# Performance work log

Measured on AMD Instinct MI355X. Metric: run time of the kernel, lower is better.

Reference implementation:

```python
import jax, jax.numpy as jnp
import numpy as np


def _log_g(x):
    # log of g(x) = where(x>=0, x+0.5, sigmoid(x)), computed stably in log-space
    return jnp.where(x >= 0, jnp.log(jax.nn.relu(x) + 0.5), -jax.nn.softplus(-x))


def setup_inputs() -> dict:
    key = jax.random.key(0)
    k1, k2, k3, k4, k5 = jax.random.split(key, 5)
    B, T, D, E = 4, 4096, 1024, 2048  # batch, seq, dim, exp_dim (expansion 2.0)
    x = jax.random.normal(k1, (B, T, D), dtype=jnp.float32)
    log_h_0 = jax.random.normal(k2, (B, 1, E), dtype=jnp.float32)
    # torch Linear(dim, 2*exp_dim): store transposed weight [D, 2E] for x @ w_f
    w_f = jax.random.normal(k3, (D, 2 * E), dtype=jnp.float32) * (1.0 / np.sqrt(D))
    b_f = jax.random.normal(k4, (2 * E,), dtype=jnp.float32) * 0.01
    # torch Linear(exp_dim, dim, bias=False): stored as [E, D] for h_t @ w_down
    w_down = jax.random.normal(k5, (E, D), dtype=jnp.float32) * (1.0 / np.sqrt(E))
    return {"x": x, "log_h_0": log_h_0, "w_f": w_f, "b_f": b_f, "w_down": w_down}


def reference(x, log_h_0, w_f, b_f, w_down):
    # fused gate/candidate projection: [B,T,2E]
    proj = jnp.einsum("btd,de->bte", x, w_f) + b_f
    k, h_x = jnp.split(proj, 2, axis=-1)  # each [B,T,E]
    log_z = -jax.nn.softplus(-k)          # log sigmoid(k)
    log_coeffs = -jax.nn.softplus(k)      # log (1 - sigmoid(k))
    log_tilde_h = _log_g(h_x)
    # prepend initial state: log_values [B,T+1,E]
    log_values = jnp.concatenate([log_h_0, log_tilde_h + log_z], axis=1)
    # a_star = pad(cumsum(log_coeffs), one leading zero along time) -> [B,T+1,E]
    a_star = jnp.pad(jnp.cumsum(log_coeffs, axis=1), ((0, 0), (1, 0), (0, 0)))
    # log-space parallel scan
    log_h = a_star + jax.lax.cumlogsumexp(log_values - a_star, axis=1)
    h_t = jnp.exp(log_h)[:, 1:]  # [B,T,E]
    h = jnp.einsum("bte,ed->btd", h_t, w_down)  # down projection (dropout p=0 -> identity)
    return h, jnp.log(h_t[:, 2:-1:3])
```

## Files before the change

kernel.cpp:

```cpp
#include <hip/hip_runtime.h>
#include <cstdint>
#include <cstddef>

typedef __attribute__((ext_vector_type(4))) float f32x4;
typedef __attribute__((ext_vector_type(8))) short short8;

__device__ __forceinline__ unsigned short f2bf(float f) {
  unsigned int u = __float_as_uint(f);
  u += 0x7fffu + ((u >> 16) & 1u);
  return (unsigned short)(u >> 16);
}
__device__ __forceinline__ float bf2f(unsigned short h) {
  return __uint_as_float(((unsigned int)h) << 16);
}

__device__ __forceinline__ void gload16(const unsigned short* g, unsigned short* l) {
  __builtin_amdgcn_global_load_lds(
      (const __attribute__((address_space(1))) void*)g,
      (__attribute__((address_space(3))) void*)l, 16, 0, 0);
}

__global__ __launch_bounds__(256) void k_cast(const float* __restrict__ src,
                                              unsigned short* __restrict__ hi) {
  size_t i = ((size_t)blockIdx.x * 256 + threadIdx.x) * 4;
  float4 v = *(const float4*)(src + i);
  *(ushort4*)(hi + i) = make_ushort4(f2bf(v.x), f2bf(v.y), f2bf(v.z), f2bf(v.w));
}

__global__ __launch_bounds__(256) void k_transpose(const float* __restrict__ src,
                                                   unsigned short* __restrict__ hi,
                                                   int R, int C) {
  __shared__ float tile[32][33];
  int tx = threadIdx.x & 31, ty = threadIdx.x >> 5;
  int c0 = blockIdx.x * 32, r0 = blockIdx.y * 32;
#pragma unroll
  for (int i = 0; i < 4; ++i)
    tile[ty + 8 * i][tx] = src[(size_t)(r0 + ty + 8 * i) * C + (c0 + tx)];
  __syncthreads();
#pragma unroll
  for (int i = 0; i < 4; ++i) {
    float v = tile[tx][ty + 8 * i];
    hi[(size_t)(c0 + ty + 8 * i) * R + (r0 + tx)] = f2bf(v);
  }
}

template<bool BF16OUT>
__global__ __launch_bounds__(512, 2) void k_gemm(const unsigned short* __restrict__ A,
                                                 const unsigned short* __restrict__ B,
                                                 void* __restrict__ Cv, int M, int N, int K) {
  __shared__ unsigned short lds[65536];
  const int tid = threadIdx.x, wave = tid >> 6, lane = tid & 63;
  const size_t row0 = (size_t)blockIdx.x * 256;
  const size_t col0 = (size_t)blockIdx.y * 256;
  const int wr = wave >> 2, wc = wave & 3;
  const int r16 = lane & 15;
  const int ksw = (lane >> 4) ^ ((r16 >> 1) & 3);
  const int aoff = (wr * 128 + r16) * 32 + ksw * 8;
  const int boff = 8192 + (wc * 64 + r16) * 32 + ksw * 8;
  const int gchunk = (tid & 3) ^ ((tid >> 3) & 3);

  f32x4 acc[8][4];
#pragma unroll
  for (int i = 0; i < 8; ++i)
#pragma unroll
    for (int j = 0; j < 4; ++j) acc[i][j] = (f32x4){0.f, 0.f, 0.f, 0.f};

  auto SREG = [&](int b, int arr, int inst, int kt) {
    const unsigned short* src = arr ? B : A;
    size_t grow = (arr ? col0 : row0) + (size_t)(inst * 128 + (tid >> 2));
    gload16(src + grow * (size_t)K + (size_t)(kt * 32 + gchunk * 8),
            &lds[(b << 14) + arr * 8192 + inst * 4096 + wave * 512]);
  };

#pragma unroll
  for (int t = 0; t < 3; ++t) {
    SREG(t, 0, 0, t); SREG(t, 0, 1, t);
    SREG(t, 1, 0, t); SREG(t, 1, 1, t);
  }

  const int nT = K >> 5;
  for (int u = 0; u < nT; ++u) {
    const unsigned short* buf = &lds[(u & 3) << 14];
    const int sb = (u + 3) & 3;
    const bool pf = (u + 3 < nT);
    const int rem = nT - 1 - u;
    if (rem >= 2)      asm volatile("s_waitcnt vmcnt(8)" ::: "memory");
    else if (rem == 1) asm volatile("s_waitcnt vmcnt(4)" ::: "memory");
    else               asm volatile("s_waitcnt vmcnt(0)" ::: "memory");
    asm volatile("s_barrier" ::: "memory");
    short8 a4[4], b4[4];
#pragma unroll
    for (int nb = 0; nb < 4; ++nb)
      b4[nb] = *(const short8*)&buf[boff + nb * 512];
#pragma unroll
    for (int mb = 0; mb < 4; ++mb)
      a4[mb] = *(const short8*)&buf[aoff + mb * 512];
    if (pf) { SREG(sb, 0, 0, u + 3); SREG(sb, 1, 0, u + 3); }
    __builtin_amdgcn_s_setprio(1);
#pragma unroll
    for (int mb = 0; mb < 4; ++mb)
#pragma unroll
      for (int nb = 0; nb < 4; ++nb)
        acc[mb][nb] = __builtin_amdgcn_mfma_f32_16x16x32_bf16(a4[mb], b4[nb], acc[mb][nb], 0, 0, 0);
    __builtin_amdgcn_s_setprio(0);
#pragma unroll
    for (int mb = 0; mb < 4; ++mb)
      a4[mb] = *(const short8*)&buf[aoff + (4 + mb) * 512];
    if (pf) { SREG(sb, 0, 1, u + 3); SREG(sb, 1, 1, u + 3); }
    __builtin_amdgcn_s_setprio(1);
#pragma unroll
    for (int mb = 0; mb < 4; ++mb)
#pragma unroll
      for (int nb = 0; nb < 4; ++nb)
        acc[4 + mb][nb] = __builtin_amdgcn_mfma_f32_16x16x32_bf16(a4[mb], b4[nb], acc[4 + mb][nb], 0, 0, 0);
    __builtin_amdgcn_s_setprio(0);
  }

#pragma unroll
  for (int m = 0; m < 8; ++m)
#pragma unroll
    for (int n = 0; n < 4; ++n) {
      size_t row = row0 + wr * 128 + m * 16 + (lane >> 4) * 4;
      size_t col = col0 + wc * 64 + n * 16 + r16;
      if (BF16OUT) {
        unsigned short* C = (unsigned short*)Cv;
#pragma unroll
        for (int r = 0; r < 4; ++r) C[(row + r) * (size_t)N + col] = f2bf(acc[m][n][r]);
      } else {
        float* C = (float*)Cv;
#pragma unroll
        for (int r = 0; r < 4; ++r) C[(row + r) * (size_t)N + col] = acc[m][n][r];
      }
    }
}

#define SB 4
#define ST 4096
#define SE 2048
#define CHUNK 64
#define NCHUNK 64
#define NCHAIN (SB * SE)

__device__ __forceinline__ void transform_lin(float k, float hx, float& c, float& v) {
  float e = __expf(-k);
  float r = __builtin_amdgcn_rcpf(1.f + e);
  c = e * r;
  float e2 = __expf(-hx);
  float sg = __builtin_amdgcn_rcpf(1.f + e2);
  float g = (hx >= 0.f) ? (hx + 0.5f) : sg;
  v = r * g;
}

__global__ __launch_bounds__(256) void k_scan1(const unsigned short* __restrict__ proj,
                                               const float* __restrict__ bfv,
                                               float* __restrict__ Ac,
                                               float* __restrict__ Bc) {
  int idx = blockIdx.x * 256 + threadIdx.x;
  int e = idx & (SE - 1), b = (idx >> 11) & 3, c = idx >> 13;
  const float bk = bfv[e], bh = bfv[SE + e];
  float A = 1.f, S = 0.f;
  size_t base = ((size_t)(b * ST + c * CHUNK) * (2 * SE)) + e;
  for (int i = 0; i < CHUNK; ++i) {
    float cc, vv;
    transform_lin(bf2f(proj[base]) + bk, bf2f(proj[base + SE]) + bh, cc, vv);
    A *= cc;
    S = fmaf(cc, S, vv);
    base += 2 * SE;
  }
  int chain = b * SE + e;
  Ac[(size_t)c * NCHAIN + chain] = A;
  Bc[(size_t)c * NCHAIN + chain] = S;
}

__global__ __launch_bounds__(256) void k_scan2(const float* __restrict__ lh0,
                                               const float* __restrict__ Ac,
                                               const float* __restrict__ Bc,
                                               float* __restrict__ Hin) {
  int chain = blockIdx.x * 256 + threadIdx.x;
  float H = __expf(lh0[chain]);
  for (int c = 0; c < NCHUNK; ++c) {
    Hin[(size_t)c * NCHAIN + chain] = H;
    H = fmaf(Ac[(size_t)c * NCHAIN + chain], H, Bc[(size_t)c * NCHAIN + chain]);
  }
}

__global__ __launch_bounds__(256) void k_scan3(const unsigned short* __restrict__ proj,
                                               const float* __restrict__ bfv,
                                               const float* __restrict__ Hin,
                                               unsigned short* __restrict__ ht,
                                               float* __restrict__ out2) {
  int idx = blockIdx.x * 256 + threadIdx.x;
  int e = idx & (SE - 1), b = (idx >> 11) & 3, c = idx >> 13;
  const float bk = bfv[e], bh = bfv[SE + e];
  float S = Hin[(size_t)c * NCHAIN + b * SE + e];
  size_t base = ((size_t)(b * ST + c * CHUNK) * (2 * SE)) + e;
  int t = c * CHUNK;
  size_t hto = ((size_t)(b * ST + t) * SE) + e;
  for (int i = 0; i < CHUNK; ++i, ++t) {
    float cc, vv;
    transform_lin(bf2f(proj[base]) + bk, bf2f(proj[base + SE]) + bh, cc, vv);
    S = fmaf(cc, S, vv);
    ht[hto] = f2bf(S);
    if (t >= 2 && ((t - 2) % 3) == 0) {
      int j = (t - 2) / 3;
      out2[((size_t)b * 1365 + j) * SE + e] = __logf(S);
    }
    base += 2 * SE;
    hto += SE;
  }
}

extern "C" void kernel_launch(void* const* d_in, const int* in_sizes, int n_in,
                              void* d_out, int out_size, void* d_ws, size_t ws_size,
                              hipStream_t stream) {
  const float* x   = (const float*)d_in[0];
  const float* lh0 = (const float*)d_in[1];
  const float* wf  = (const float*)d_in[2];
  const float* bfv = (const float*)d_in[3];
  const float* wd  = (const float*)d_in[4];
  float* out1 = (float*)d_out;
  float* out2 = out1 + (size_t)SB * ST * 1024;

  char* p = (char*)d_ws;
  unsigned short* proj = (unsigned short*)p; p += 16384ull * 4096 * 2;
  unsigned short* xhi  = (unsigned short*)p; p += 16384ull * 1024 * 2;
  unsigned short* wfh  = (unsigned short*)p; p += 4096ull * 1024 * 2;
  unsigned short* wdt  = (unsigned short*)p; p += 1024ull * 2048 * 2;
  unsigned short* ht   = (unsigned short*)p; p += 16384ull * 2048 * 2;
  float* Ac            = (float*)p;          p += 64ull * 8192 * 4;
  float* Bc            = (float*)p;          p += 64ull * 8192 * 4;
  float* Hin           = (float*)p;          p += 64ull * 8192 * 4;

  hipLaunchKernelGGL(k_cast, dim3(16384), dim3(256), 0, stream, x, xhi);
  hipLaunchKernelGGL(k_transpose, dim3(128, 32), dim3(256), 0, stream, wf, wfh, 1024, 4096);
  hipLaunchKernelGGL(k_transpose, dim3(32, 64),  dim3(256), 0, stream, wd, wdt, 2048, 1024);
  hipLaunchKernelGGL((k_gemm<true>), dim3(64, 16), dim3(512), 0, stream,
                     xhi, wfh, (void*)proj, 16384, 4096, 1024);
  hipLaunchKernelGGL(k_scan1, dim3(2048), dim3(256), 0, stream, proj, bfv, Ac, Bc);
  hipLaunchKernelGGL(k_scan2, dim3(32), dim3(256), 0, stream, lh0, Ac, Bc, Hin);
  hipLaunchKernelGGL(k_scan3, dim3(2048), dim3(256), 0, stream, proj, bfv, Hin, ht, out2);
  hipLaunchKernelGGL((k_gemm<false>), dim3(64, 4), dim3(512), 0, stream,
                     ht, wdt, (void*)out1, 16384, 1024, 2048);
}
```

Before: 319.4 us.

## Interleave gate and candidate weight columns and fuse prep kernels into one launch

The w_f transpose now interleaves k and h_x columns, so the projection GEMM writes each gate/candidate pair as adjacent bf16 values. The scan kernels can then fetch both with one 32-bit load instead of two strided 16-bit loads. Biases are packed into a float2 array. The cast and two transposes are merged into a single launch to save launch overhead, at the cost of a branchy kernel whose blocks shared memory with mixed roles.

```diff
diff --git a/kernel.cpp b/kernel.cpp
--- a/kernel.cpp
+++ b/kernel.cpp
@@ -13,6 +13,12 @@
 __device__ __forceinline__ float bf2f(unsigned short h) {
   return __uint_as_float(((unsigned int)h) << 16);
 }
+__device__ __forceinline__ float bflo(unsigned int w) {
+  return __uint_as_float(w << 16);
+}
+__device__ __forceinline__ float bfhi(unsigned int w) {
+  return __uint_as_float(w & 0xffff0000u);
+}
 
 __device__ __forceinline__ void gload16(const unsigned short* g, unsigned short* l) {
   __builtin_amdgcn_global_load_lds(
@@ -20,28 +26,57 @@
       (__attribute__((address_space(3))) void*)l, 16, 0, 0);
 }
 
-__global__ __launch_bounds__(256) void k_cast(const float* __restrict__ src,
-                                              unsigned short* __restrict__ hi) {
-  size_t i = ((size_t)blockIdx.x * 256 + threadIdx.x) * 4;
-  float4 v = *(const float4*)(src + i);
-  *(ushort4*)(hi + i) = make_ushort4(f2bf(v.x), f2bf(v.y), f2bf(v.z), f2bf(v.w));
-}
-
-__global__ __launch_bounds__(256) void k_transpose(const float* __restrict__ src,
-                                                   unsigned short* __restrict__ hi,
-                                                   int R, int C) {
-  __shared__ float tile[32][33];
-  int tx = threadIdx.x & 31, ty = threadIdx.x >> 5;
-  int c0 = blockIdx.x * 32, r0 = blockIdx.y * 32;
-#pragma unroll
-  for (int i = 0; i < 4; ++i)
-    tile[ty + 8 * i][tx] = src[(size_t)(r0 + ty + 8 * i) * C + (c0 + tx)];
-  __syncthreads();
-#pragma unroll
-  for (int i = 0; i < 4; ++i) {
-    float v = tile[tx][ty + 8 * i];
-    hi[(size_t)(c0 + ty + 8 * i) * R + (r0 + tx)] = f2bf(v);
-  }
+__global__ __launch_bounds__(256) void k_prep(const float* __restrict__ x,
+                                              unsigned short* __restrict__ xhi,
+                                              const float* __restrict__ wf,
+                                              unsigned short* __restrict__ wfh,
+                                              const float* __restrict__ wd,
+                                              unsigned short* __restrict__ wdt,
+                                              const float* __restrict__ bfv,
+                                              float2* __restrict__ bfi) {
+  int blk = blockIdx.x;
+  if (blk < 16384) {
+    size_t i = ((size_t)blk * 256 + threadIdx.x) * 4;
+    float4 v = *(const float4*)(x + i);
+    *(ushort4*)(xhi + i) = make_ushort4(f2bf(v.x), f2bf(v.y), f2bf(v.z), f2bf(v.w));
+    return;
+  }
+  blk -= 16384;
+  if (blk < 4096) {
+    __shared__ float tile[32][33];
+    int tx = threadIdx.x & 31, ty = threadIdx.x >> 5;
+    int bx = blk & 127, by = blk >> 7;
+    int c0 = bx * 32, r0 = by * 32;
+#pragma unroll
+    for (int i = 0; i < 4; ++i)
+      tile[ty + 8 * i][tx] = wf[(size_t)(r0 + ty + 8 * i) * 4096 + (c0 + tx)];
+    __syncthreads();
+#pragma unroll
+    for (int i = 0; i < 4; ++i) {
+      int j = c0 + ty + 8 * i;
+      int r = (j < 2048) ? (2 * j) : (2 * (j - 2048) + 1);
+      wfh[(size_t)r * 1024 + (r0 + tx)] = f2bf(tile[tx][ty + 8 * i]);
+    }
+    return;
+  }
+  blk -= 4096;
+  if (blk < 2048) {
+    __shared__ float tile[32][33];
+    int tx = threadIdx.x & 31, ty = threadIdx.x >> 5;
+    int bx = blk & 31, by = blk >> 5;
+    int c0 = bx * 32, r0 = by * 32;
+#pragma unroll
+    for (int i = 0; i < 4; ++i)
+      tile[ty + 8 * i][tx] = wd[(size_t)(r0 + ty + 8 * i) * 1024 + (c0 + tx)];
+    __syncthreads();
+#pragma unroll
+    for (int i = 0; i < 4; ++i)
+      wdt[(size_t)(c0 + ty + 8 * i) * 2048 + (r0 + tx)] = f2bf(tile[tx][ty + 8 * i]);
+    return;
+  }
+  blk -= 2048;
+  int i = blk * 256 + threadIdx.x;
+  if (i < 2048) bfi[i] = make_float2(bfv[i], bfv[2048 + i]);
 }
 
 template<bool BF16OUT>
@@ -151,21 +186,22 @@
   v = r * g;
 }
 
-__global__ __launch_bounds__(256) void k_scan1(const unsigned short* __restrict__ proj,
-                                               const float* __restrict__ bfv,
+__global__ __launch_bounds__(256) void k_scan1(const unsigned int* __restrict__ proj32,
+                                               const float2* __restrict__ bfi,
                                                float* __restrict__ Ac,
                                                float* __restrict__ Bc) {
   int idx = blockIdx.x * 256 + threadIdx.x;
   int e = idx & (SE - 1), b = (idx >> 11) & 3, c = idx >> 13;
-  const float bk = bfv[e], bh = bfv[SE + e];
+  const float2 bb = bfi[e];
   float A = 1.f, S = 0.f;
-  size_t base = ((size_t)(b * ST + c * CHUNK) * (2 * SE)) + e;
+  size_t base = ((size_t)(b * ST + c * CHUNK)) * SE + e;
   for (int i = 0; i < CHUNK; ++i) {
+    unsigned int w = proj32[base];
     float cc, vv;
-    transform_lin(bf2f(proj[base]) + bk, bf2f(proj[base + SE]) + bh, cc, vv);
+    transform_lin(bflo(w) + bb.x, bfhi(w) + bb.y, cc, vv);
     A *= cc;
     S = fmaf(cc, S, vv);
-    base += 2 * SE;
+    base += SE;
   }
   int chain = b * SE + e;
   Ac[(size_t)c * NCHAIN + chain] = A;
@@ -184,28 +220,29 @@
   }
 }
 
-__global__ __launch_bounds__(256) void k_scan3(const unsigned short* __restrict__ proj,
-                                               const float* __restrict__ bfv,
+__global__ __launch_bounds__(256) void k_scan3(const unsigned int* __restrict__ proj32,
+                                               const float2* __restrict__ bfi,
                                                const float* __restrict__ Hin,
                                                unsigned short* __restrict__ ht,
                                                float* __restrict__ out2) {
   int idx = blockIdx.x * 256 + threadIdx.x;
   int e = idx & (SE - 1), b = (idx >> 11) & 3, c = idx >> 13;
-  const float bk = bfv[e], bh = bfv[SE + e];
+  const float2 bb = bfi[e];
   float S = Hin[(size_t)c * NCHAIN + b * SE + e];
-  size_t base = ((size_t)(b * ST + c * CHUNK) * (2 * SE)) + e;
+  size_t base = ((size_t)(b * ST + c * CHUNK)) * SE + e;
   int t = c * CHUNK;
-  size_t hto = ((size_t)(b * ST + t) * SE) + e;
+  size_t hto = ((size_t)(b * ST + t)) * SE + e;
   for (int i = 0; i < CHUNK; ++i, ++t) {
+    unsigned int w = proj32[base];
     float cc, vv;
-    transform_lin(bf2f(proj[base]) + bk, bf2f(proj[base + SE]) + bh, cc, vv);
+    transform_lin(bflo(w) + bb.x, bfhi(w) + bb.y, cc, vv);
     S = fmaf(cc, S, vv);
     ht[hto] = f2bf(S);
     if (t >= 2 && ((t - 2) % 3) == 0) {
       int j = (t - 2) / 3;
       out2[((size_t)b * 1365 + j) * SE + e] = __logf(S);
     }
-    base += 2 * SE;
+    base += SE;
     hto += SE;
   }
 }
@@ -230,15 +267,17 @@
   float* Ac            = (float*)p;          p += 64ull * 8192 * 4;
   float* Bc            = (float*)p;          p += 64ull * 8192 * 4;
   float* Hin           = (float*)p;          p += 64ull * 8192 * 4;
-
-  hipLaunchKernelGGL(k_cast, dim3(16384), dim3(256), 0, stream, x, xhi);
-  hipLaunchKernelGGL(k_transpose, dim3(128, 32), dim3(256), 0, stream, wf, wfh, 1024, 4096);
-  hipLaunchKernelGGL(k_transpose, dim3(32, 64),  dim3(256), 0, stream, wd, wdt, 2048, 1024);
+  float2* bfi          = (float2*)p;         p += 2048ull * 8;
+
+  hipLaunchKernelGGL(k_prep, dim3(16384 + 4096 + 2048 + 8), dim3(256), 0, stream,
+                     x, xhi, wf, wfh, wd, wdt, bfv, bfi);
   hipLaunchKernelGGL((k_gemm<true>), dim3(64, 16), dim3(512), 0, stream,
                      xhi, wfh, (void*)proj, 16384, 4096, 1024);
-  hipLaunchKernelGGL(k_scan1, dim3(2048), dim3(256), 0, stream, proj, bfv, Ac, Bc);
+  hipLaunchKernelGGL(k_scan1, dim3(2048), dim3(256), 0, stream,
+                     (const unsigned int*)proj, bfi, Ac, Bc);
   hipLaunchKernelGGL(k_scan2, dim3(32), dim3(256), 0, stream, lh0, Ac, Bc, Hin);
-  hipLaunchKernelGGL(k_scan3, dim3(2048), dim3(256), 0, stream, proj, bfv, Hin, ht, out2);
+  hipLaunchKernelGGL(k_scan3, dim3(2048), dim3(256), 0, stream,
+                     (const unsigned int*)proj, bfi, Hin, ht, out2);
   hipLaunchKernelGGL((k_gemm<false>), dim3(64, 4), dim3(512), 0, stream,
                      ht, wdt, (void*)out1, 16384, 1024, 2048);
 }
```

Result: faster. 309.0 us (-3.2%).
